# Optimization experiments

Hardware: AMD Instinct MI355X
Metric: run time of the kernel (lower is better)

## Reference

```python
import jax, jax.numpy as jnp
import numpy as np

N, E, D = 100000, 1000000, 128  # nodes, edges, feature/embedding dim


def setup_inputs() -> dict:
    key = jax.random.key(0)
    ks = jax.random.split(key, 8)
    s = 1.0 / np.sqrt(D)
    return {
        "x": jax.random.normal(ks[0], (N, D), jnp.float32),
        "edge_index": jax.random.randint(ks[1], (2, E), 0, N, jnp.int32),
        # layer 1: lin_l (with bias) on aggregated neighbors, lin_r (no bias) on root
        "W1_l": jax.random.normal(ks[2], (D, D), jnp.float32) * s,
        "b1_l": jnp.zeros((D,), jnp.float32),
        "W1_r": jax.random.normal(ks[3], (D, D), jnp.float32) * s,
        # layer 2
        "W2_l": jax.random.normal(ks[4], (D, D), jnp.float32) * s,
        "b2_l": jnp.zeros((D,), jnp.float32),
        "W2_r": jax.random.normal(ks[5], (D, D), jnp.float32) * s,
    }


def _sage_conv(x, src, dst, Wl, bl, Wr):
    # PyG SAGEConv (aggr='mean'): out = lin_l(mean_{j->i} x_j) + lin_r(x_i)
    msgs = x[src]                                            # [E, D] gather
    agg = jax.ops.segment_sum(msgs, dst, num_segments=N)     # [N, D] scatter-add
    cnt = jax.ops.segment_sum(jnp.ones((src.shape[0],), x.dtype), dst,
                              num_segments=N)                # [N]
    mean = agg / jnp.maximum(cnt, 1.0)[:, None]
    return mean @ Wl + bl + x @ Wr


def reference(x, edge_index, W1_l, b1_l, W1_r, W2_l, b2_l, W2_r):
    src, dst = edge_index[0], edge_index[1]
    h = jax.nn.relu(_sage_conv(x, src, dst, W1_l, b1_l, W1_r))  # dropout inactive (eval)
    return _sage_conv(h, src, dst, W2_l, b2_l, W2_r)            # [N, D] embeddings
```

## Files before the change

### kernel.cpp

```cpp
#include <hip/hip_runtime.h>

#define D 128
constexpr int NPB   = 128;
constexpr int BCAP  = 1536;
constexpr int SEGB  = 2048;
constexpr int KMAX  = 1024;

typedef __bf16 bf16x8 __attribute__((ext_vector_type(8)));
typedef float f32x4 __attribute__((ext_vector_type(4)));
typedef int intv4 __attribute__((ext_vector_type(4)));

__device__ __forceinline__ unsigned short f2bf(float f) {
    unsigned int u = __float_as_uint(f);
    unsigned int r = (u + 0x7fffu + ((u >> 16) & 1u)) >> 16;
    return (unsigned short)r;
}
__device__ __forceinline__ unsigned pack2(float a, float b) {
    return (unsigned)f2bf(a) | ((unsigned)f2bf(b) << 16);
}
__device__ __forceinline__ int q8clamp(float v) {
    int q = __float2int_rn(v);
    return min(max(q, -127), 127);
}

__global__ __launch_bounds__(256) void front_kernel(
    const int* __restrict__ src, const int* __restrict__ dst,
    unsigned long long* __restrict__ bucket, int* __restrict__ bCur,
    int E, int K, int NB,
    const float* __restrict__ W1l, const float* __restrict__ W1r,
    const float* __restrict__ W2l, const float* __restrict__ W2r,
    unsigned short* __restrict__ Wpack,
    const float* __restrict__ xin, unsigned short* __restrict__ xb,
    unsigned* __restrict__ xq, float* __restrict__ sx, int n4)
{
    const int t = threadIdx.x;
    if (blockIdx.x < (unsigned)NB) {
        __shared__ int lcnt[KMAX], lbase[KMAX];
        for (int i = t; i < K; i += 256) lcnt[i] = 0;
        __syncthreads();

        const int e0 = blockIdx.x * SEGB + t * 8;
        intv4 d0, d1, s0, s1;
        if (e0 + 8 <= E) {
            d0 = __builtin_nontemporal_load(reinterpret_cast<const intv4*>(dst + e0));
            d1 = __builtin_nontemporal_load(reinterpret_cast<const intv4*>(dst + e0 + 4));
            s0 = __builtin_nontemporal_load(reinterpret_cast<const intv4*>(src + e0));
            s1 = __builtin_nontemporal_load(reinterpret_cast<const intv4*>(src + e0 + 4));
        } else {
#pragma unroll
            for (int k = 0; k < 4; ++k) {
                d0[k] = (e0 + k < E) ? dst[e0 + k] : -1;
                d1[k] = (e0 + 4 + k < E) ? dst[e0 + 4 + k] : -1;
                s0[k] = (e0 + k < E) ? src[e0 + k] : 0;
                s1[k] = (e0 + 4 + k < E) ? src[e0 + 4 + k] : 0;
            }
        }
#pragma unroll
        for (int k = 0; k < 8; ++k) {
            int d = (k < 4) ? d0[k] : d1[k - 4];
            if (d >= 0) atomicAdd(&lcnt[d >> 7], 1);
        }
        __syncthreads();
        for (int i = t; i < K; i += 256) {
            int c = lcnt[i];
            lbase[i] = c ? atomicAdd(&bCur[i], c) : 0;
            lcnt[i] = 0;
        }
        __syncthreads();
#pragma unroll
        for (int k = 0; k < 8; ++k) {
            int d = (k < 4) ? d0[k] : d1[k - 4];
            int s = (k < 4) ? s0[k] : s1[k - 4];
            if (d >= 0) {
                int b = d >> 7;
                int p = lbase[b] + atomicAdd(&lcnt[b], 1);
                if (p < BCAP)
                    bucket[(size_t)b * BCAP + p] =
                        ((unsigned long long)(unsigned)s << 32) | (unsigned)d;
            }
        }
    } else if (blockIdx.x < (unsigned)(NB + 32)) {
        int b = (blockIdx.x - NB) * 4 + (t >> 6);
        int l = t & 63;
        int layer = b >> 6, wsel = (b >> 5) & 1, kt = (b >> 3) & 3, ct = b & 7;
        const float* W = layer ? (wsel ? W2r : W2l) : (wsel ? W1r : W1l);
        int k0  = kt * 32 + (l >> 4) * 8;
        int col = ct * 16 + (l & 15);
        unsigned short tmp[8];
#pragma unroll
        for (int j = 0; j < 8; ++j) tmp[j] = f2bf(W[(k0 + j) * D + col]);
        size_t fbase = (((size_t)layer * 64 + wsel * 32 + kt * 8 + ct) * 64 + l) * 8;
        uint4 o;
        o.x = (unsigned)tmp[0] | ((unsigned)tmp[1] << 16);
        o.y = (unsigned)tmp[2] | ((unsigned)tmp[3] << 16);
        o.z = (unsigned)tmp[4] | ((unsigned)tmp[5] << 16);
        o.w = (unsigned)tmp[6] | ((unsigned)tmp[7] << 16);
        *reinterpret_cast<uint4*>(Wpack + fbase) = o;
    } else {
        int i = (blockIdx.x - NB - 32) * 256 + t;
        if (i < n4) {
            float4 v = reinterpret_cast<const float4*>(xin)[i];
            ushort4 o;
            o.x = f2bf(v.x); o.y = f2bf(v.y); o.z = f2bf(v.z); o.w = f2bf(v.w);
            reinterpret_cast<ushort4*>(xb)[i] = o;
            float am = fmaxf(fmaxf(fabsf(v.x), fabsf(v.y)),
                             fmaxf(fabsf(v.z), fabsf(v.w)));
#pragma unroll
            for (int off = 1; off < 32; off <<= 1)
                am = fmaxf(am, __shfl_xor(am, off, 32));
            am = fmaxf(am, 1e-20f);
            float inv = 127.0f / am;
            unsigned q = ((unsigned)(q8clamp(v.x * inv) & 0xff))
                       | ((unsigned)(q8clamp(v.y * inv) & 0xff) << 8)
                       | ((unsigned)(q8clamp(v.z * inv) & 0xff) << 16)
                       | ((unsigned)(q8clamp(v.w * inv) & 0xff) << 24);
            xq[i] = q;
            if ((t & 31) == 0) sx[i >> 5] = am / 127.0f;
        }
    }
}

__global__ __launch_bounds__(256) void csrbuild_kernel(
    const unsigned long long* __restrict__ bucket, const int* __restrict__ bCur,
    int2* __restrict__ offe, int* __restrict__ csr, int K, int N)
{
    __shared__ unsigned long long ebuf[BCAP];
    __shared__ int lhist[NPB], sc[NPB], lcur[NPB];
    __shared__ int red[256];
    const int t = threadIdx.x;
    const int b = blockIdx.x;

    int s = 0;
    for (int i = t; i < b; i += 256) s += bCur[i];
    red[t] = s;
    __syncthreads();
    for (int o = 128; o; o >>= 1) {
        if (t < o) red[t] += red[t + o];
        __syncthreads();
    }
    const int gbase = red[0];
    const int cnt = min(bCur[b], BCAP);

    if (t < NPB) lhist[t] = 0;
    __syncthreads();

    const unsigned long long* bp = bucket + (size_t)b * BCAP;
    for (int i = t; i < cnt; i += 256) {
        unsigned long long e = bp[i];
        ebuf[i] = e;
        atomicAdd(&lhist[(int)(e & 127ULL)], 1);
    }
    __syncthreads();

    if (t < NPB) sc[t] = lhist[t];
    __syncthreads();
    for (int o = 1; o < NPB; o <<= 1) {
        int y = 0;
        if (t < NPB && t >= o) y = sc[t - o];
        __syncthreads();
        if (t < NPB) sc[t] += y;
        __syncthreads();
    }
    if (t < NPB) {
        int node = b * NPB + t;
        int excl = sc[t] - lhist[t];
        lcur[t] = excl;
        if (node < N) offe[node] = make_int2(gbase + excl, gbase + sc[t]);
    }
    __syncthreads();

    for (int i = t; i < cnt; i += 256) {
        unsigned long long e = ebuf[i];
        int dl = (int)(e & 127ULL);
        int p = gbase + atomicAdd(&lcur[dl], 1);
        csr[p] = (int)(e >> 32);
    }
}

__global__ __launch_bounds__(256) void quantH_kernel(
    const unsigned short* __restrict__ hb, uint2* __restrict__ hq,
    float* __restrict__ sh, int N)
{
    int idx = blockIdx.x * 256 + threadIdx.x;
    int n = idx >> 4;
    int q = idx & 15;
    if (n >= N) return;
    uint4 v = *reinterpret_cast<const uint4*>(hb + (size_t)n * D + q * 8);
    const unsigned* u = &v.x;
    float f[8];
#pragma unroll
    for (int i = 0; i < 4; ++i) {
        f[2 * i]     = __uint_as_float(u[i] << 16);
        f[2 * i + 1] = __uint_as_float(u[i] & 0xffff0000u);
    }
    float am = 0.f;
#pragma unroll
    for (int i = 0; i < 8; ++i) am = fmaxf(am, fabsf(f[i]));
#pragma unroll
    for (int off = 1; off < 16; off <<= 1)
        am = fmaxf(am, __shfl_xor(am, off, 16));
    am = fmaxf(am, 1e-20f);
    float inv = 127.0f / am;
    uint2 o;
    o.x = ((unsigned)(q8clamp(f[0] * inv) & 0xff))
        | ((unsigned)(q8clamp(f[1] * inv) & 0xff) << 8)
        | ((unsigned)(q8clamp(f[2] * inv) & 0xff) << 16)
        | ((unsigned)(q8clamp(f[3] * inv) & 0xff) << 24);
    o.y = ((unsigned)(q8clamp(f[4] * inv) & 0xff))
        | ((unsigned)(q8clamp(f[5] * inv) & 0xff) << 8)
        | ((unsigned)(q8clamp(f[6] * inv) & 0xff) << 16)
        | ((unsigned)(q8clamp(f[7] * inv) & 0xff) << 24);
    hq[(size_t)n * 16 + q] = o;
    if (q == 0) sh[n] = am / 127.0f;
}

__device__ __forceinline__ void acc8(uint2 v, float sc, float* acc) {
#pragma unroll
    for (int w = 0; w < 2; ++w) {
        unsigned x = w ? v.y : v.x;
#pragma unroll
        for (int b = 0; b < 4; ++b) {
            int e = (int)((signed char)((x >> (8 * b)) & 0xffu));
            acc[4 * w + b] = fmaf((float)e, sc, acc[4 * w + b]);
        }
    }
}

__global__ __launch_bounds__(256) void gather8_i8(
    const uint2* __restrict__ q8, const float* __restrict__ scales,
    const int2* __restrict__ offe, const int* __restrict__ csr,
    unsigned short* __restrict__ mean, int N)
{
    int tid = blockIdx.x * 256 + threadIdx.x;
    int n   = tid >> 4;
    int q   = tid & 15;
    if (n >= N) return;
    int2 be = offe[n];
    int b = be.x, e = be.y;
    const uint2* fp = q8 + q;

    float acc[8];
#pragma unroll
    for (int i = 0; i < 8; ++i) acc[i] = 0.f;

    int j = b;
    for (; j + 3 < e; j += 4) {
        int s0 = __builtin_nontemporal_load(csr + j);
        int s1 = __builtin_nontemporal_load(csr + j + 1);
        int s2 = __builtin_nontemporal_load(csr + j + 2);
        int s3 = __builtin_nontemporal_load(csr + j + 3);
        uint2 v0 = fp[(size_t)s0 * 16];
        uint2 v1 = fp[(size_t)s1 * 16];
        uint2 v2 = fp[(size_t)s2 * 16];
        uint2 v3 = fp[(size_t)s3 * 16];
        float c0 = scales[s0];
        float c1 = scales[s1];
        float c2 = scales[s2];
        float c3 = scales[s3];
        acc8(v0, c0, acc);
        acc8(v1, c1, acc);
        acc8(v2, c2, acc);
        acc8(v3, c3, acc);
    }
    for (; j < e; ++j) {
        int s0 = csr[j];
        uint2 v0 = fp[(size_t)s0 * 16];
        acc8(v0, scales[s0], acc);
    }
    float invd = 1.0f / (float)max(e - b, 1);
#pragma unroll
    for (int i = 0; i < 8; ++i) acc[i] *= invd;
    uint4 o;
    o.x = pack2(acc[0], acc[1]);
    o.y = pack2(acc[2], acc[3]);
    o.z = pack2(acc[4], acc[5]);
    o.w = pack2(acc[6], acc[7]);
    *reinterpret_cast<uint4*>(mean + (size_t)n * D + q * 8) = o;
}

template <int RELU, int OUT_BF16>
__global__ __launch_bounds__(256, 2) void sage_mfma(
    const unsigned short* __restrict__ meanb,
    const unsigned short* __restrict__ xb,
    const unsigned short* __restrict__ Wpack,
    const float* __restrict__ bl,
    void* __restrict__ outv, int Mtiles, int TPB)
{
    __shared__ __align__(16) char sbuf[2][8192];
    const int t    = threadIdx.x;
    const int lane = t & 63;
    const int wc   = t >> 6;
    const int l15  = lane & 15;
    const int lhi  = lane >> 4;

    bf16x8 bfrag[2][8];
#pragma unroll
    for (int ktt = 0; ktt < 8; ++ktt) {
        int wsel = ktt >> 2, kt = ktt & 3;
#pragma unroll
        for (int c = 0; c < 2; ++c) {
            int ct = wc * 2 + c;
            size_t fbase = ((size_t)(wsel * 32 + kt * 8 + ct) * 64 + lane) * 8;
            bfrag[c][ktt] = *reinterpret_cast<const bf16x8*>(Wpack + fbase);
        }
    }
    float bias[2];
    bias[0] = bl[wc * 32 + l15];
    bias[1] = bl[wc * 32 + 16 + l15];

    int tile0 = blockIdx.x * TPB;
    if (tile0 >= Mtiles) return;
    int tend = min(tile0 + TPB, Mtiles);

    const int sr = t >> 4;
    const int sq = t & 15;
    const int ss = sq ^ (sr & 7);
    char* dstM = &sbuf[0][sr * 256 + ss * 16];
    char* dstX = &sbuf[0][4096 + sr * 256 + ss * 16];

    {
        size_t gofs = (size_t)(tile0 * 16 + sr) * D + sq * 8;
        *reinterpret_cast<uint4*>(dstM) = *reinterpret_cast<const uint4*>(meanb + gofs);
        *reinterpret_cast<uint4*>(dstX) = *reinterpret_cast<const uint4*>(xb + gofs);
    }
    int cur = 0;

    for (int it = tile0; it < tend; ++it) {
        __syncthreads();
        const bool pf = (it + 1 < tend);
        uint4 mv, xv;
        if (pf) {
            size_t gofs = (size_t)((it + 1) * 16 + sr) * D + sq * 8;
            mv = *reinterpret_cast<const uint4*>(meanb + gofs);
            xv = *reinterpret_cast<const uint4*>(xb + gofs);
        }

        f32x4 acc0 = {0.f, 0.f, 0.f, 0.f};
        f32x4 acc1 = {0.f, 0.f, 0.f, 0.f};
        const char* base = sbuf[cur];
#pragma unroll
        for (int ktt = 0; ktt < 8; ++ktt) {
            int p = ktt >> 2, kt = ktt & 3;
            int q = kt * 4 + lhi;
            int byteoff = p * 4096 + l15 * 256 + ((q ^ (l15 & 7)) * 16);
            bf16x8 a = *reinterpret_cast<const bf16x8*>(base + byteoff);
            acc0 = __builtin_amdgcn_mfma_f32_16x16x32_bf16(a, bfrag[0][ktt], acc0, 0, 0, 0);
            acc1 = __builtin_amdgcn_mfma_f32_16x16x32_bf16(a, bfrag[1][ktt], acc1, 0, 0, 0);
        }

        int rbase = it * 16 + lhi * 4;
#pragma unroll
        for (int c = 0; c < 2; ++c) {
            int col = wc * 32 + c * 16 + l15;
            const f32x4& a = c ? acc1 : acc0;
#pragma unroll
            for (int r = 0; r < 4; ++r) {
                float v = a[r] + bias[c];
                if (RELU) v = fmaxf(v, 0.f);
                if (OUT_BF16) {
                    ((unsigned short*)outv)[(size_t)(rbase + r) * D + col] = f2bf(v);
                } else {
                    ((float*)outv)[(size_t)(rbase + r) * D + col] = v;
                }
            }
        }

        if (pf) {
            char* dM = dstM + (cur ^ 1) * 8192;
            char* dX = dstX + (cur ^ 1) * 8192;
            *reinterpret_cast<uint4*>(dM) = mv;
            *reinterpret_cast<uint4*>(dX) = xv;
            cur ^= 1;
        }
    }
}

extern "C" void kernel_launch(void* const* d_in, const int* in_sizes, int n_in,
                              void* d_out, int out_size, void* d_ws, size_t ws_size,
                              hipStream_t stream) {
    const float* x   = (const float*)d_in[0];
    const int*   ei  = (const int*)d_in[1];
    const float* W1l = (const float*)d_in[2];
    const float* b1l = (const float*)d_in[3];
    const float* W1r = (const float*)d_in[4];
    const float* W2l = (const float*)d_in[5];
    const float* b2l = (const float*)d_in[6];
    const float* W2r = (const float*)d_in[7];
    float* out = (float*)d_out;

    const int N = in_sizes[0] / D;
    const int E = in_sizes[1] / 2;
    const int* src = ei;
    const int* dst = ei + E;

    const int K = (N + NPB - 1) / NPB;

    unsigned short* xb    = (unsigned short*)d_ws;
    unsigned short* meanb = xb + (size_t)N * D;
    unsigned short* hb    = meanb + (size_t)N * D;
    unsigned short* Wpack = hb + (size_t)N * D;
    int* bCur     = (int*)(Wpack + 65536);
    int2* offe    = (int2*)(bCur + KMAX);
    int* csr_src  = (int*)(offe + N);
    float* sx     = (float*)(csr_src + E);
    float* sh     = sx + N;

    unsigned long long* bucket = (unsigned long long*)hb;
    unsigned* xq = (unsigned*)((char*)hb + (size_t)K * BCAP * 8);
    uint2* hq = (uint2*)xb;

    const int Mtiles  = (N + 15) / 16;
    const int TPB     = 8;
    const int gemmGrid = (Mtiles + TPB - 1) / TPB;
    const int gatherBlocks = (int)(((long long)N * 16 + 255) / 256);
    const int NB = (E + SEGB - 1) / SEGB;
    const int n4 = N * D / 4;
    const int convBlocks = (n4 + 255) / 256;
    const int quantBlocks = (int)(((long long)N * 16 + 255) / 256);

    hipMemsetAsync(bCur, 0, (size_t)K * sizeof(int), stream);
    front_kernel<<<NB + 32 + convBlocks, 256, 0, stream>>>(
        src, dst, bucket, bCur, E, K, NB,
        W1l, W1r, W2l, W2r, Wpack, x, xb, xq, sx, n4);
    csrbuild_kernel<<<K, 256, 0, stream>>>(bucket, bCur, offe, csr_src, K, N);

    gather8_i8<<<gatherBlocks, 256, 0, stream>>>(
        (const uint2*)xq, sx, offe, csr_src, meanb, N);
    sage_mfma<1, 1><<<gemmGrid, 256, 0, stream>>>(meanb, xb, Wpack, b1l, hb, Mtiles, TPB);

    quantH_kernel<<<quantBlocks, 256, 0, stream>>>(hb, hq, sh, N);

    gather8_i8<<<gatherBlocks, 256, 0, stream>>>(
        hq, sh, offe, csr_src, meanb, N);
    sage_mfma<0, 0><<<gemmGrid, 256, 0, stream>>>(meanb, hb, Wpack + 32768, b2l, out, Mtiles, TPB);
}
```

Before: 161.5 us.

## Fuse int8 quantization of hidden layer into GEMM epilogue; enlarge bucketing segment

Removes the separate quantH kernel by computing per-row absmax and int8 quantization of h directly in the layer-1 MFMA epilogue. Row maxima are combined with shuffles and shared-memory atomicMax, which adds extra block syncs per tile. The quantized output goes to its own workspace region instead of aliasing xb. Separately, the edge bucketing pass now gives each block 8192 edges instead of 2048, so fewer blocks do global atomics, at the cost of more registers per thread.

New measurement: 149.8 us. -7.2%, faster.

```diff
diff --git a/kernel.cpp b/kernel.cpp
--- a/kernel.cpp
+++ b/kernel.cpp
@@ -3,7 +3,7 @@
 #define D 128
 constexpr int NPB   = 128;
 constexpr int BCAP  = 1536;
-constexpr int SEGB  = 2048;
+constexpr int SEGB  = 8192;
 constexpr int KMAX  = 1024;
 
 typedef __bf16 bf16x8 __attribute__((ext_vector_type(8)));
@@ -39,26 +39,30 @@
         for (int i = t; i < K; i += 256) lcnt[i] = 0;
         __syncthreads();
 
-        const int e0 = blockIdx.x * SEGB + t * 8;
-        intv4 d0, d1, s0, s1;
-        if (e0 + 8 <= E) {
-            d0 = __builtin_nontemporal_load(reinterpret_cast<const intv4*>(dst + e0));
-            d1 = __builtin_nontemporal_load(reinterpret_cast<const intv4*>(dst + e0 + 4));
-            s0 = __builtin_nontemporal_load(reinterpret_cast<const intv4*>(src + e0));
-            s1 = __builtin_nontemporal_load(reinterpret_cast<const intv4*>(src + e0 + 4));
-        } else {
-#pragma unroll
-            for (int k = 0; k < 4; ++k) {
-                d0[k] = (e0 + k < E) ? dst[e0 + k] : -1;
-                d1[k] = (e0 + 4 + k < E) ? dst[e0 + 4 + k] : -1;
-                s0[k] = (e0 + k < E) ? src[e0 + k] : 0;
-                s1[k] = (e0 + 4 + k < E) ? src[e0 + 4 + k] : 0;
-            }
-        }
-#pragma unroll
-        for (int k = 0; k < 8; ++k) {
-            int d = (k < 4) ? d0[k] : d1[k - 4];
-            if (d >= 0) atomicAdd(&lcnt[d >> 7], 1);
+        const int base = blockIdx.x * SEGB;
+        intv4 dreg[8], sreg[8];
+#pragma unroll
+        for (int c = 0; c < 4; ++c) {
+            int e0 = base + c * 2048 + t * 8;
+            if (e0 + 8 <= E) {
+                dreg[2*c]   = __builtin_nontemporal_load(reinterpret_cast<const intv4*>(dst + e0));
+                dreg[2*c+1] = __builtin_nontemporal_load(reinterpret_cast<const intv4*>(dst + e0 + 4));
+                sreg[2*c]   = __builtin_nontemporal_load(reinterpret_cast<const intv4*>(src + e0));
+                sreg[2*c+1] = __builtin_nontemporal_load(reinterpret_cast<const intv4*>(src + e0 + 4));
+            } else {
+#pragma unroll
+                for (int k = 0; k < 4; ++k) {
+                    dreg[2*c][k]   = (e0 + k < E) ? dst[e0 + k] : -1;
+                    dreg[2*c+1][k] = (e0 + 4 + k < E) ? dst[e0 + 4 + k] : -1;
+                    sreg[2*c][k]   = (e0 + k < E) ? src[e0 + k] : 0;
+                    sreg[2*c+1][k] = (e0 + 4 + k < E) ? src[e0 + 4 + k] : 0;
+                }
+            }
+#pragma unroll
+            for (int k = 0; k < 8; ++k) {
+                int d = dreg[2*c + (k >> 2)][k & 3];
+                if (d >= 0) atomicAdd(&lcnt[d >> 7], 1);
+            }
         }
         __syncthreads();
         for (int i = t; i < K; i += 256) {
@@ -68,15 +72,18 @@
         }
         __syncthreads();
 #pragma unroll
-        for (int k = 0; k < 8; ++k) {
-            int d = (k < 4) ? d0[k] : d1[k - 4];
-            int s = (k < 4) ? s0[k] : s1[k - 4];
-            if (d >= 0) {
-                int b = d >> 7;
-                int p = lbase[b] + atomicAdd(&lcnt[b], 1);
-                if (p < BCAP)
-                    bucket[(size_t)b * BCAP + p] =
-                        ((unsigned long long)(unsigned)s << 32) | (unsigned)d;
+        for (int c = 0; c < 4; ++c) {
+#pragma unroll
+            for (int k = 0; k < 8; ++k) {
+                int d = dreg[2*c + (k >> 2)][k & 3];
+                int s = sreg[2*c + (k >> 2)][k & 3];
+                if (d >= 0) {
+                    int b = d >> 7;
+                    int p = lbase[b] + atomicAdd(&lcnt[b], 1);
+                    if (p < BCAP)
+                        bucket[(size_t)b * BCAP + p] =
+                            ((unsigned long long)(unsigned)s << 32) | (unsigned)d;
+                }
             }
         }
     } else if (blockIdx.x < (unsigned)(NB + 32)) {
@@ -175,43 +182,6 @@
         int p = gbase + atomicAdd(&lcur[dl], 1);
         csr[p] = (int)(e >> 32);
     }
-}
-
-__global__ __launch_bounds__(256) void quantH_kernel(
-    const unsigned short* __restrict__ hb, uint2* __restrict__ hq,
-    float* __restrict__ sh, int N)
-{
-    int idx = blockIdx.x * 256 + threadIdx.x;
-    int n = idx >> 4;
-    int q = idx & 15;
-    if (n >= N) return;
-    uint4 v = *reinterpret_cast<const uint4*>(hb + (size_t)n * D + q * 8);
-    const unsigned* u = &v.x;
-    float f[8];
-#pragma unroll
-    for (int i = 0; i < 4; ++i) {
-        f[2 * i]     = __uint_as_float(u[i] << 16);
-        f[2 * i + 1] = __uint_as_float(u[i] & 0xffff0000u);
-    }
-    float am = 0.f;
-#pragma unroll
-    for (int i = 0; i < 8; ++i) am = fmaxf(am, fabsf(f[i]));
-#pragma unroll
-    for (int off = 1; off < 16; off <<= 1)
-        am = fmaxf(am, __shfl_xor(am, off, 16));
-    am = fmaxf(am, 1e-20f);
-    float inv = 127.0f / am;
-    uint2 o;
-    o.x = ((unsigned)(q8clamp(f[0] * inv) & 0xff))
-        | ((unsigned)(q8clamp(f[1] * inv) & 0xff) << 8)
-        | ((unsigned)(q8clamp(f[2] * inv) & 0xff) << 16)
-        | ((unsigned)(q8clamp(f[3] * inv) & 0xff) << 24);
-    o.y = ((unsigned)(q8clamp(f[4] * inv) & 0xff))
-        | ((unsigned)(q8clamp(f[5] * inv) & 0xff) << 8)
-        | ((unsigned)(q8clamp(f[6] * inv) & 0xff) << 16)
-        | ((unsigned)(q8clamp(f[7] * inv) & 0xff) << 24);
-    hq[(size_t)n * 16 + q] = o;
-    if (q == 0) sh[n] = am / 127.0f;
 }
 
 __device__ __forceinline__ void acc8(uint2 v, float sc, float* acc) {
@@ -278,15 +248,18 @@
     *reinterpret_cast<uint4*>(mean + (size_t)n * D + q * 8) = o;
 }
 
-template <int RELU, int OUT_BF16>
+template <int RELU, int OUT_BF16, int QUANT>
 __global__ __launch_bounds__(256, 2) void sage_mfma(
     const unsigned short* __restrict__ meanb,
     const unsigned short* __restrict__ xb,
     const unsigned short* __restrict__ Wpack,
     const float* __restrict__ bl,
-    void* __restrict__ outv, int Mtiles, int TPB)
+    void* __restrict__ outv,
+    signed char* __restrict__ hq, float* __restrict__ sh,
+    int Mtiles, int TPB)
 {
     __shared__ __align__(16) char sbuf[2][8192];
+    __shared__ int rowmaxI[16];
     const int t    = threadIdx.x;
     const int lane = t & 63;
     const int wc   = t >> 6;
@@ -349,19 +322,59 @@
         }
 
         int rbase = it * 16 + lhi * 4;
+        float v[2][4];
+#pragma unroll
+        for (int c = 0; c < 2; ++c) {
+            const f32x4& a = c ? acc1 : acc0;
+#pragma unroll
+            for (int r = 0; r < 4; ++r) {
+                float w = a[r] + bias[c];
+                if (RELU) w = fmaxf(w, 0.f);
+                v[c][r] = w;
+            }
+        }
 #pragma unroll
         for (int c = 0; c < 2; ++c) {
             int col = wc * 32 + c * 16 + l15;
-            const f32x4& a = c ? acc1 : acc0;
 #pragma unroll
             for (int r = 0; r < 4; ++r) {
-                float v = a[r] + bias[c];
-                if (RELU) v = fmaxf(v, 0.f);
                 if (OUT_BF16) {
-                    ((unsigned short*)outv)[(size_t)(rbase + r) * D + col] = f2bf(v);
+                    ((unsigned short*)outv)[(size_t)(rbase + r) * D + col] = f2bf(v[c][r]);
                 } else {
-                    ((float*)outv)[(size_t)(rbase + r) * D + col] = v;
+                    ((float*)outv)[(size_t)(rbase + r) * D + col] = v[c][r];
                 }
+            }
+        }
+
+        if (QUANT) {
+            float m[4];
+#pragma unroll
+            for (int r = 0; r < 4; ++r) m[r] = fmaxf(v[0][r], v[1][r]);
+#pragma unroll
+            for (int mask = 1; mask < 16; mask <<= 1)
+#pragma unroll
+                for (int r = 0; r < 4; ++r)
+                    m[r] = fmaxf(m[r], __shfl_xor(m[r], mask, 64));
+            __syncthreads();
+            if (t < 16) rowmaxI[t] = 0;
+            __syncthreads();
+            if (l15 == 0) {
+#pragma unroll
+                for (int r = 0; r < 4; ++r)
+                    atomicMax(&rowmaxI[lhi * 4 + r], __float_as_int(m[r]));
+            }
+            __syncthreads();
+#pragma unroll
+            for (int r = 0; r < 4; ++r) {
+                float rm = __int_as_float(rowmaxI[lhi * 4 + r]);
+                float inv = 127.0f / fmaxf(rm, 1e-20f);
+                int row = rbase + r;
+#pragma unroll
+                for (int c = 0; c < 2; ++c) {
+                    int col = wc * 32 + c * 16 + l15;
+                    hq[(size_t)row * D + col] = (signed char)q8clamp(v[c][r] * inv);
+                }
+                if (wc == 0 && l15 == 0) sh[row] = rm / 127.0f;
             }
         }
 
@@ -404,10 +417,10 @@
     int* csr_src  = (int*)(offe + N);
     float* sx     = (float*)(csr_src + E);
     float* sh     = sx + N;
+    signed char* hq = (signed char*)(sh + N);
 
     unsigned long long* bucket = (unsigned long long*)hb;
     unsigned* xq = (unsigned*)((char*)hb + (size_t)K * BCAP * 8);
-    uint2* hq = (uint2*)xb;
 
     const int Mtiles  = (N + 15) / 16;
     const int TPB     = 8;
@@ -416,7 +429,6 @@
     const int NB = (E + SEGB - 1) / SEGB;
     const int n4 = N * D / 4;
     const int convBlocks = (n4 + 255) / 256;
-    const int quantBlocks = (int)(((long long)N * 16 + 255) / 256);
 
     hipMemsetAsync(bCur, 0, (size_t)K * sizeof(int), stream);
     front_kernel<<<NB + 32 + convBlocks, 256, 0, stream>>>(
@@ -426,11 +438,11 @@
 
     gather8_i8<<<gatherBlocks, 256, 0, stream>>>(
         (const uint2*)xq, sx, offe, csr_src, meanb, N);
-    sage_mfma<1, 1><<<gemmGrid, 256, 0, stream>>>(meanb, xb, Wpack, b1l, hb, Mtiles, TPB);
-
-    quantH_kernel<<<quantBlocks, 256, 0, stream>>>(hb, hq, sh, N);
+    sage_mfma<1, 1, 1><<<gemmGrid, 256, 0, stream>>>(
+        meanb, xb, Wpack, b1l, hb, hq, sh, Mtiles, TPB);
 
     gather8_i8<<<gatherBlocks, 256, 0, stream>>>(
-        hq, sh, offe, csr_src, meanb, N);
-    sage_mfma<0, 0><<<gemmGrid, 256, 0, stream>>>(meanb, hb, Wpack + 32768, b2l, out, Mtiles, TPB);
-}
+        (const uint2*)hq, sh, offe, csr_src, meanb, N);
+    sage_mfma<0, 0, 0><<<gemmGrid, 256, 0, stream>>>(
+        meanb, hb, Wpack + 32768, b2l, out, nullptr, nullptr, Mtiles, TPB);
+}
```
